# Optimization experiments

Measured on AMD Instinct MI355X. Metric: run time of the kernel, lower is better.

The kernel has to match this reference:

```python
import jax, jax.numpy as jnp
import numpy as np

H = 1024      # hidden_size
NH = 16       # num_heads
DK = H // NH  # head dim


def setup_inputs() -> dict:
    key = jax.random.key(0)
    ks = jax.random.split(key, 5)
    s = 0.02
    return {
        "x": jax.random.normal(ks[0], (4, 2048, H), dtype=jnp.float32),
        "W_attn": jax.random.normal(ks[1], (H, 3 * H), dtype=jnp.float32) * s,
        "b_attn": jnp.zeros((3 * H,), dtype=jnp.float32),
        "W_proj": jax.random.normal(ks[2], (H, H), dtype=jnp.float32) * s,
        "b_proj": jnp.zeros((H,), dtype=jnp.float32),
    }


def reference(x, W_attn, b_attn, W_proj, b_proj):
    B, S, _ = x.shape
    qkv = x @ W_attn + b_attn                      # [B,S,3H]
    q, k, v = jnp.split(qkv, 3, axis=-1)
    # split heads -> [B,NH,S,DK]
    def heads(t):
        return t.reshape(B, S, NH, DK).transpose(0, 2, 1, 3)
    q, k, v = heads(q), heads(k), heads(v)
    scores = jnp.einsum("bhqd,bhkd->bhqk", q, k) / jnp.sqrt(jnp.float32(DK))
    causal = jnp.triu(jnp.full((S, S), -jnp.inf, dtype=scores.dtype), k=1)
    scores = scores + causal                        # additive causal mask
    attn = jax.nn.softmax(scores, axis=-1)
    out = jnp.einsum("bhqk,bhkd->bhqd", attn, v)   # [B,NH,S,DK]
    out = out.transpose(0, 2, 1, 3).reshape(B, S, H)
    return out @ W_proj + b_proj
```

## Files before the change

### kernel.cpp

```cpp
#include <hip/hip_runtime.h>
#include <hip/hip_bf16.h>


typedef __attribute__((ext_vector_type(8))) short bhalf8;
typedef __attribute__((ext_vector_type(4))) float floatx4;
typedef __attribute__((ext_vector_type(16))) float floatx16;

#define SB 2048
#define HB 1024
#define H3 3072

#if __has_builtin(__builtin_amdgcn_exp2f)
#define EXP2(x) __builtin_amdgcn_exp2f(x)
#else
#define EXP2(x) exp2f(x)
#endif

__device__ __forceinline__ float bf2f(unsigned short u) {
  union { unsigned int i; float f; } c; c.i = ((unsigned int)u) << 16; return c.f;
}
__device__ __forceinline__ unsigned short f2bf(float f) {
  union { float f; unsigned int i; } c; c.f = f;
  unsigned int r = c.i + 0x7fffu + ((c.i >> 16) & 1u);
  return (unsigned short)(r >> 16);
}
__device__ __forceinline__ int pkbf(float lo, float hi_) {
  union { __hip_bfloat162 h; int i; } u;
  u.h = __float22bfloat162_rn(make_float2(lo, hi_));
  return u.i;
}

__device__ __forceinline__ void gl_lds16(const unsigned short* g, unsigned short* l) {
  __builtin_amdgcn_global_load_lds(
      (const __attribute__((address_space(1))) unsigned int*)g,
      (__attribute__((address_space(3))) unsigned int*)l, 16, 0, 0);
}

#define REP16(OP) OP(0) OP(1) OP(2) OP(3) OP(4) OP(5) OP(6) OP(7) \
                  OP(8) OP(9) OP(10) OP(11) OP(12) OP(13) OP(14) OP(15)

__global__ void cvt_f32_bf16(const float* __restrict__ in, unsigned short* __restrict__ out, int n) {
  int i = (blockIdx.x * blockDim.x + threadIdx.x) * 4;
  if (i >= n) return;
  float4 v = *(const float4*)(in + i);
  ushort4 o;
  o.x = f2bf(v.x); o.y = f2bf(v.y); o.z = f2bf(v.z); o.w = f2bf(v.w);
  *(ushort4*)(out + i) = o;
}

__global__ void transpose_cvt(const float* __restrict__ in, unsigned short* __restrict__ out,
                              int K, int N) {
  __shared__ float tile[32][33];
  int n0 = blockIdx.x * 32, k0 = blockIdx.y * 32;
  for (int i = threadIdx.y; i < 32; i += 8)
    tile[i][threadIdx.x] = in[(size_t)(k0 + i) * N + n0 + threadIdx.x];
  __syncthreads();
  for (int i = threadIdx.y; i < 32; i += 8)
    out[(size_t)(n0 + i) * K + k0 + threadIdx.x] = f2bf(tile[threadIdx.x][i]);
}

__global__ void transpose_v(const unsigned short* __restrict__ qkv,
                            unsigned short* __restrict__ Vt) {
  __shared__ unsigned short tile[32][33];
  const int bh = blockIdx.z;
  const int b = bh >> 4, h = bh & 15;
  const int s0 = blockIdx.x * 32;
  const int d0 = blockIdx.y * 32;
  const int tx = threadIdx.x;
  const unsigned short* src = qkv + (size_t)(b * SB + s0) * H3 + 2 * HB + h * 64 + d0;
  for (int i = threadIdx.y; i < 32; i += 8)
    tile[i][tx] = src[(size_t)i * H3 + tx];
  __syncthreads();
  unsigned short* dst = Vt + ((size_t)bh * 64 + d0) * SB + s0;
  for (int i = threadIdx.y; i < 32; i += 8)
    dst[(size_t)i * SB + tx] = tile[tx][i];
}

__global__ __launch_bounds__(512, 2) void gemm_v8(
    const unsigned short* __restrict__ A,
    const unsigned short* __restrict__ Bt,
    const float* __restrict__ bias,
    unsigned short* __restrict__ C,
    int M, int N, int K) {
  __shared__ __align__(16) unsigned short Sm[3 * 20480];
  const int tid = threadIdx.x;
  const int lane = tid & 63;
  const int w = tid >> 6;
  const int l15 = lane & 15, l4 = lane >> 4;
  const int wm = w >> 2, wn = w & 3;

  const int gx = gridDim.x;
  int lin = blockIdx.y * gx + blockIdx.x;
  const int cpx = (gx * gridDim.y) >> 3;
  lin = (lin & 7) * cpx + (lin >> 3);
  const int m0 = (lin / gx) * 256;
  const int n0 = (lin % gx) * 384;

  const int rb0 = tid >> 2;
  const int co = (((tid & 3) ^ ((tid >> 3) & 3)) * 8);
  const unsigned short* pA0 = A + (size_t)(m0 + rb0) * K + co;
  const unsigned short* pA1 = pA0 + (size_t)128 * K;
  const unsigned short* pB0 = Bt + (size_t)(n0 + rb0) * K + co;
  const unsigned short* pB1 = pB0 + (size_t)128 * K;
  const unsigned short* pB2 = pB0 + (size_t)256 * K;

  const int ra0 = wm * 128 + l15;
  const int ab0 = ra0 * 64 + ((l4 ^ ((ra0 >> 1) & 3)) << 4);
  const int rbq = wn * 96 + l15;
  const int bb0 = 16384 + rbq * 64 + ((l4 ^ ((rbq >> 1) & 3)) << 4);

  const floatx4 zero = {0.f, 0.f, 0.f, 0.f};
  floatx4 acc[8][6];
#pragma unroll
  for (int i = 0; i < 8; ++i)
#pragma unroll
    for (int j = 0; j < 6; ++j) acc[i][j] = zero;

#define STAGE_A(k0, ss)                                                 \
  { gl_lds16(pA0 + (k0), Sm + (ss) + tid * 8);                          \
    gl_lds16(pA1 + (k0), Sm + (ss) + (tid + 512) * 8); }
#define STAGE_B(k0, ss)                                                 \
  { gl_lds16(pB0 + (k0), Sm + (ss) + 8192 + tid * 8);                   \
    gl_lds16(pB1 + (k0), Sm + (ss) + 8192 + (tid + 512) * 8);           \
    gl_lds16(pB2 + (k0), Sm + (ss) + 8192 + (tid + 1024) * 8); }

  const int NT = K >> 5;
  STAGE_A(0, 0)      STAGE_B(0, 0)
  STAGE_A(32, 20480) STAGE_B(32, 20480)
  int sb = 0;
  int ss = 40960;

  for (int t = 0; t < NT; ++t) {
    if (t < NT - 1) asm volatile("s_waitcnt vmcnt(5)" ::: "memory");
    else            asm volatile("s_waitcnt vmcnt(0)" ::: "memory");
    __builtin_amdgcn_s_barrier();

    const char* LB = (const char*)(Sm + sb);
    const int k2 = (t + 2) * 32;
    const bool st = (t + 2 < NT);

    bhalf8 a0 = *(const bhalf8*)(LB + ab0);
    bhalf8 a1 = *(const bhalf8*)(LB + ab0 + 1024);
    bhalf8 a2 = *(const bhalf8*)(LB + ab0 + 2048);
    bhalf8 a3 = *(const bhalf8*)(LB + ab0 + 3072);
    bhalf8 b0 = *(const bhalf8*)(LB + bb0);
    bhalf8 b1 = *(const bhalf8*)(LB + bb0 + 1024);
    bhalf8 b2 = *(const bhalf8*)(LB + bb0 + 2048);
    bhalf8 b3 = *(const bhalf8*)(LB + bb0 + 3072);
    bhalf8 b4 = *(const bhalf8*)(LB + bb0 + 4096);
    bhalf8 b5 = *(const bhalf8*)(LB + bb0 + 5120);
    if (st) STAGE_A(k2, ss)
    asm volatile("s_waitcnt lgkmcnt(0)" ::: "memory");
    __builtin_amdgcn_sched_barrier(0);
    __builtin_amdgcn_s_setprio(1);
#define MROW(i, av)                                                              \
    acc[i][0] = __builtin_amdgcn_mfma_f32_16x16x32_bf16(av, b0, acc[i][0], 0, 0, 0); \
    acc[i][1] = __builtin_amdgcn_mfma_f32_16x16x32_bf16(av, b1, acc[i][1], 0, 0, 0); \
    acc[i][2] = __builtin_amdgcn_mfma_f32_16x16x32_bf16(av, b2, acc[i][2], 0, 0, 0); \
    acc[i][3] = __builtin_amdgcn_mfma_f32_16x16x32_bf16(av, b3, acc[i][3], 0, 0, 0); \
    acc[i][4] = __builtin_amdgcn_mfma_f32_16x16x32_bf16(av, b4, acc[i][4], 0, 0, 0); \
    acc[i][5] = __builtin_amdgcn_mfma_f32_16x16x32_bf16(av, b5, acc[i][5], 0, 0, 0);
    MROW(0, a0) MROW(1, a1) MROW(2, a2) MROW(3, a3)
    __builtin_amdgcn_s_setprio(0);
    __builtin_amdgcn_sched_barrier(0);
    __builtin_amdgcn_s_barrier();

    bhalf8 a4 = *(const bhalf8*)(LB + ab0 + 4096);
    bhalf8 a5 = *(const bhalf8*)(LB + ab0 + 5120);
    bhalf8 a6 = *(const bhalf8*)(LB + ab0 + 6144);
    bhalf8 a7 = *(const bhalf8*)(LB + ab0 + 7168);
    if (st) STAGE_B(k2, ss)
    asm volatile("s_waitcnt lgkmcnt(0)" ::: "memory");
    __builtin_amdgcn_sched_barrier(0);
    __builtin_amdgcn_s_setprio(1);
    MROW(4, a4) MROW(5, a5) MROW(6, a6) MROW(7, a7)
#undef MROW
    __builtin_amdgcn_s_setprio(0);
    __builtin_amdgcn_sched_barrier(0);
    __builtin_amdgcn_s_barrier();

    sb = (sb == 40960) ? 0 : sb + 20480;
    ss = (ss == 40960) ? 0 : ss + 20480;
  }
#undef STAGE_A
#undef STAGE_B

#pragma unroll
  for (int i = 0; i < 8; ++i) {
    int row = m0 + wm * 128 + i * 16 + (l4 << 2);
#pragma unroll
    for (int j = 0; j < 6; ++j) {
      int col = n0 + wn * 96 + j * 16 + l15;
      float bb = bias[col];
#pragma unroll
      for (int r = 0; r < 4; ++r)
        C[(size_t)(row + r) * N + col] = f2bf(acc[i][j][r] + bb);
    }
  }
}

template <bool F32OUT>
__global__ __launch_bounds__(512, 4) void gemm_v6(
    const unsigned short* __restrict__ A,
    const unsigned short* __restrict__ Bt,
    const float* __restrict__ bias,
    void* __restrict__ Cv,
    int M, int N, int K) {
  __shared__ __align__(16) unsigned short Sm[3 * 12288];
  const int tid = threadIdx.x;
  const int lane = tid & 63;
  const int w = tid >> 6;
  const int l15 = lane & 15, l4 = lane >> 4;
  const int wr = (w >> 1) * 64;
  const int wc = (w & 1) * 64;

  const int gx = gridDim.x;
  int lin = blockIdx.y * gx + blockIdx.x;
  const int cpx = (gx * gridDim.y) >> 3;
  lin = (lin & 7) * cpx + (lin >> 3);
  const int m0 = (lin / gx) * 256;
  const int n0 = (lin % gx) * 128;

  const int idx0 = tid, idx1 = tid + 512;
  const unsigned short* pA0 = A + (size_t)(m0 + (idx0 >> 2)) * K + (((idx0 & 3) ^ ((idx0 >> 3) & 3)) * 8);
  const unsigned short* pA1 = A + (size_t)(m0 + (idx1 >> 2)) * K + (((idx1 & 3) ^ ((idx1 >> 3) & 3)) * 8);
  const unsigned short* pB  = Bt + (size_t)(n0 + (tid >> 2)) * K + (((tid & 3) ^ ((tid >> 3) & 3)) * 8);

  int abyte[4], bbyte[4];
#pragma unroll
  for (int i = 0; i < 4; ++i) {
    int ra = wr + i * 16 + l15;
    abyte[i] = ra * 64 + ((l4 ^ ((ra >> 1) & 3)) << 4);
    int rb = wc + i * 16 + l15;
    bbyte[i] = 16384 + rb * 64 + ((l4 ^ ((rb >> 1) & 3)) << 4);
  }

  const floatx4 zero = {0.f, 0.f, 0.f, 0.f};
  floatx4 acc[4][4];
#pragma unroll
  for (int i = 0; i < 4; ++i)
#pragma unroll
    for (int j = 0; j < 4; ++j) acc[i][j] = zero;

#define STAGE_A6(k0, sbase)                                             \
  { gl_lds16(pA0 + (k0), Sm + (sbase) + idx0 * 8);                      \
    gl_lds16(pA1 + (k0), Sm + (sbase) + idx1 * 8); }
#define STAGE_B6(k0, sbase)                                             \
  { gl_lds16(pB + (k0), Sm + (sbase) + 8192 + tid * 8); }

  const int NT = K >> 5;
  STAGE_A6(0, 0)  STAGE_B6(0, 0)
  STAGE_A6(32, 12288) STAGE_B6(32, 12288)
  int sb = 0;
  int ss = 24576;

  for (int t = 0; t < NT; ++t) {
    if (t < NT - 1) asm volatile("s_waitcnt vmcnt(3)" ::: "memory");
    else            asm volatile("s_waitcnt vmcnt(0)" ::: "memory");
    __builtin_amdgcn_s_barrier();

    const char* LB = (const char*)(Sm + sb);
    const int k2 = (t + 2) * 32;
    const bool st = (t + 2 < NT);

    bhalf8 a0 = *(const bhalf8*)(LB + abyte[0]);
    bhalf8 a1 = *(const bhalf8*)(LB + abyte[1]);
    bhalf8 b0 = *(const bhalf8*)(LB + bbyte[0]);
    bhalf8 b1 = *(const bhalf8*)(LB + bbyte[1]);
    bhalf8 b2 = *(const bhalf8*)(LB + bbyte[2]);
    bhalf8 b3 = *(const bhalf8*)(LB + bbyte[3]);
    if (st) STAGE_A6(k2, ss)
    asm volatile("s_waitcnt lgkmcnt(0)" ::: "memory");
    __builtin_amdgcn_sched_barrier(0);
    __builtin_amdgcn_s_setprio(1);
    acc[0][0] = __builtin_amdgcn_mfma_f32_16x16x32_bf16(a0, b0, acc[0][0], 0, 0, 0);
    acc[0][1] = __builtin_amdgcn_mfma_f32_16x16x32_bf16(a0, b1, acc[0][1], 0, 0, 0);
    acc[0][2] = __builtin_amdgcn_mfma_f32_16x16x32_bf16(a0, b2, acc[0][2], 0, 0, 0);
    acc[0][3] = __builtin_amdgcn_mfma_f32_16x16x32_bf16(a0, b3, acc[0][3], 0, 0, 0);
    acc[1][0] = __builtin_amdgcn_mfma_f32_16x16x32_bf16(a1, b0, acc[1][0], 0, 0, 0);
    acc[1][1] = __builtin_amdgcn_mfma_f32_16x16x32_bf16(a1, b1, acc[1][1], 0, 0, 0);
    acc[1][2] = __builtin_amdgcn_mfma_f32_16x16x32_bf16(a1, b2, acc[1][2], 0, 0, 0);
    acc[1][3] = __builtin_amdgcn_mfma_f32_16x16x32_bf16(a1, b3, acc[1][3], 0, 0, 0);
    __builtin_amdgcn_s_setprio(0);
    __builtin_amdgcn_sched_barrier(0);
    __builtin_amdgcn_s_barrier();

    bhalf8 a2 = *(const bhalf8*)(LB + abyte[2]);
    bhalf8 a3 = *(const bhalf8*)(LB + abyte[3]);
    if (st) STAGE_B6(k2, ss)
    asm volatile("s_waitcnt lgkmcnt(0)" ::: "memory");
    __builtin_amdgcn_sched_barrier(0);
    __builtin_amdgcn_s_setprio(1);
    acc[2][0] = __builtin_amdgcn_mfma_f32_16x16x32_bf16(a2, b0, acc[2][0], 0, 0, 0);
    acc[2][1] = __builtin_amdgcn_mfma_f32_16x16x32_bf16(a2, b1, acc[2][1], 0, 0, 0);
    acc[2][2] = __builtin_amdgcn_mfma_f32_16x16x32_bf16(a2, b2, acc[2][2], 0, 0, 0);
    acc[2][3] = __builtin_amdgcn_mfma_f32_16x16x32_bf16(a2, b3, acc[2][3], 0, 0, 0);
    acc[3][0] = __builtin_amdgcn_mfma_f32_16x16x32_bf16(a3, b0, acc[3][0], 0, 0, 0);
    acc[3][1] = __builtin_amdgcn_mfma_f32_16x16x32_bf16(a3, b1, acc[3][1], 0, 0, 0);
    acc[3][2] = __builtin_amdgcn_mfma_f32_16x16x32_bf16(a3, b2, acc[3][2], 0, 0, 0);
    acc[3][3] = __builtin_amdgcn_mfma_f32_16x16x32_bf16(a3, b3, acc[3][3], 0, 0, 0);
    __builtin_amdgcn_s_setprio(0);
    __builtin_amdgcn_sched_barrier(0);
    __builtin_amdgcn_s_barrier();

    sb = (sb == 24576) ? 0 : sb + 12288;
    ss = (ss == 24576) ? 0 : ss + 12288;
  }
#undef STAGE_A6
#undef STAGE_B6

  float* Cf = (float*)Cv;
  unsigned short* Cb = (unsigned short*)Cv;
#pragma unroll
  for (int i = 0; i < 4; ++i) {
    int row = m0 + wr + i * 16 + (l4 << 2);
#pragma unroll
    for (int j = 0; j < 4; ++j) {
      int col = n0 + wc + j * 16 + l15;
      float bb = bias[col];
#pragma unroll
      for (int r = 0; r < 4; ++r) {
        float v = acc[i][j][r] + bb;
        size_t idx = (size_t)(row + r) * N + col;
        if constexpr (F32OUT) Cf[idx] = v;
        else Cb[idx] = f2bf(v);
      }
    }
  }
}

__global__ __launch_bounds__(256, 4) void flash_attn4(
    const unsigned short* __restrict__ qkv,
    const unsigned short* __restrict__ Vt,
    unsigned short* __restrict__ outp) {
  __shared__ __align__(16) unsigned short Sm[4 * 4096];

  const int tid = threadIdx.x;
  const int lane = tid & 63;
  const int w = tid >> 6;
  const int hi = lane >> 5;
  const int qc = lane & 31;
  const int bh = blockIdx.x;
  const int b = bh >> 4, h = bh & 15;
  const int qt = 15 - (int)blockIdx.y;
  const int wq0 = qt * 128 + w * 32;
  const size_t rowbase = (size_t)b * SB;
  const int qg = wq0 + qc;
  const int nt = 2 * qt + 2;

  bhalf8 qf[4];
  {
    const unsigned short* qp = qkv + (rowbase + qg) * H3 + h * 64 + hi * 8;
#pragma unroll
    for (int kk = 0; kk < 4; ++kk) {
      bhalf8 v = *(const bhalf8*)(qp + kk * 16);
      bhalf8 o;
#pragma unroll
      for (int j = 0; j < 8; ++j)
        o[j] = (short)f2bf(bf2f((unsigned short)v[j]) * 0.18033688f);
      qf[kk] = o;
    }
  }

  const floatx16 Z16 = {0,0,0,0,0,0,0,0,0,0,0,0,0,0,0,0};
  floatx16 acc0 = Z16, acc1 = Z16;
  float l_half = 0.f;

  const char* LB = (const char*)Sm;
  int koff[8];
#pragma unroll
  for (int kk = 0; kk < 4; ++kk) {
    int xo = (((2 * kk + hi) ^ (qc & 7)) << 4);
    koff[2 * kk]     = qc * 128 + xo;
    koff[2 * kk + 1] = (32 + qc) * 128 + xo;
  }

  const int srow = tid >> 3, schk = tid & 7;
  const int sxe = (schk ^ (srow & 7)) * 8;
  const unsigned short* kp = qkv + (rowbase + srow) * H3 + HB + h * 64 + sxe;
  const unsigned short* vp = Vt + ((size_t)bh * 64 + srow) * SB + sxe;

  {
    unsigned short* kb = Sm + tid * 8;
    gl_lds16(kp, kb);
    gl_lds16(kp + 32 * H3, kb + 2048);
    gl_lds16(vp, kb + 8192);
    gl_lds16(vp + 32 * SB, kb + 8192 + 2048);
  }

#define QKK(BUFB, kk)                                                              \
      { bhalf8 ka = *(const bhalf8*)(LB + (BUFB) + koff[2*(kk)]);                  \
        s0 = __builtin_amdgcn_mfma_f32_32x32x16_bf16(ka, qf[kk], s0, 0, 0, 0);     \
        bhalf8 kb2 = *(const bhalf8*)(LB + (BUFB) + koff[2*(kk)+1]);               \
        s1 = __builtin_amdgcn_mfma_f32_32x32x16_bf16(kb2, qf[kk], s1, 0, 0, 0); }
#define PVC(BUFB, c, pfv)                                                          \
      { bhalf8 va = *(const bhalf8*)(LB + 16384 + (BUFB) + koff[2*(c)]);           \
        acc0 = __builtin_amdgcn_mfma_f32_32x32x16_bf16(va, pfv, acc0, 0, 0, 0);    \
        bhalf8 vb2 = *(const bhalf8*)(LB + 16384 + (BUFB) + koff[2*(c)+1]);        \
        acc1 = __builtin_amdgcn_mfma_f32_32x32x16_bf16(vb2, pfv, acc1, 0, 0, 0); }
#define MSK0(r) { if (k0 + (((r)&3) + 8*((r)>>2)) + 4*hi > qg)      s0[r] = -3.0e38f; }
#define MSK1(r) { if (k0 + 32 + (((r)&3) + 8*((r)>>2)) + 4*hi > qg) s1[r] = -3.0e38f; }
#define PEXP(r) { s0[r] = EXP2(s0[r]); s1[r] = EXP2(s1[r]); rsx[(r)&3] += s0[r] + s1[r]; }
  union PW { int i[4]; bhalf8 v; };
#define PACK2(dst, sv, rb)                                               \
      { int A0 = pkbf(sv[rb + 0], sv[rb + 1]);                           \
        int A1 = pkbf(sv[rb + 2], sv[rb + 3]);                           \
        int B0 = pkbf(sv[rb + 4], sv[rb + 5]);                           \
        int B1 = pkbf(sv[rb + 6], sv[rb + 7]);                           \
        auto r0 = __builtin_amdgcn_permlane32_swap(A0, B0, false, false);\
        auto r1 = __builtin_amdgcn_permlane32_swap(A1, B1, false, false);\
        PW u;                                                            \
        u.i[0] = r0[0]; u.i[1] = r1[0];                                  \
        u.i[2] = r0[1]; u.i[3] = r1[1];                                  \
        dst = u.v; }

#define FLASH_COMPUTE(BUFB)                                                        \
    { floatx16 s0 = Z16, s1 = Z16;                                                 \
      __builtin_amdgcn_s_setprio(1);                                               \
      QKK(BUFB, 0) QKK(BUFB, 1) QKK(BUFB, 2) QKK(BUFB, 3)                          \
      __builtin_amdgcn_s_setprio(0);                                               \
      if (k0 + 63 > wq0) { REP16(MSK0) REP16(MSK1) }                               \
      float rsx[4] = {0.f, 0.f, 0.f, 0.f};                                         \
      REP16(PEXP)                                                                  \
      l_half += (rsx[0] + rsx[1]) + (rsx[2] + rsx[3]);                             \
      bhalf8 pf0, pf1, pf2, pf3;                                                   \
      PACK2(pf0, s0, 0) PACK2(pf1, s0, 8) PACK2(pf2, s1, 0) PACK2(pf3, s1, 8)      \
      __builtin_amdgcn_s_setprio(1);                                               \
      PVC(BUFB, 0, pf0) PVC(BUFB, 1, pf1) PVC(BUFB, 2, pf2) PVC(BUFB, 3, pf3)      \
      __builtin_amdgcn_s_setprio(0); }

#define DO_STEP(T, BUF)                                                            \
  { __syncthreads();                                                               \
    if ((T) + 1 < nt) {                                                            \
      kp += 64 * H3; vp += 64;                                                     \
      unsigned short* kb = Sm + (1 - (BUF)) * 4096 + tid * 8;                      \
      gl_lds16(kp, kb); gl_lds16(kp + 32 * H3, kb + 2048);                         \
      gl_lds16(vp, kb + 8192); gl_lds16(vp + 32 * SB, kb + 8192 + 2048);           \
    }                                                                              \
    const int k0 = (T) * 64;                                                       \
    if (k0 <= wq0 + 31) FLASH_COMPUTE((BUF) * 8192)                                \
  }

  for (int t = 0; t < nt; t += 2) {
    DO_STEP(t, 0)
    DO_STEP(t + 1, 1)
  }

  const float l_full = l_half + __shfl_xor(l_half, 32);
  const float inv_l = 1.f / l_full;
  unsigned short* op = outp + (rowbase + qg) * HB + h * 64;
#pragma unroll
  for (int tq = 0; tq < 4; ++tq) {
    ushort4 st;
    st.x = f2bf(acc0[4 * tq + 0] * inv_l);
    st.y = f2bf(acc0[4 * tq + 1] * inv_l);
    st.z = f2bf(acc0[4 * tq + 2] * inv_l);
    st.w = f2bf(acc0[4 * tq + 3] * inv_l);
    *(ushort4*)(op + 8 * tq + 4 * hi) = st;
    ushort4 su;
    su.x = f2bf(acc1[4 * tq + 0] * inv_l);
    su.y = f2bf(acc1[4 * tq + 1] * inv_l);
    su.z = f2bf(acc1[4 * tq + 2] * inv_l);
    su.w = f2bf(acc1[4 * tq + 3] * inv_l);
    *(ushort4*)(op + 32 + 8 * tq + 4 * hi) = su;
  }
}

extern "C" void kernel_launch(void* const* d_in, const int* in_sizes, int n_in,
                              void* d_out, int out_size, void* d_ws, size_t ws_size,
                              hipStream_t stream) {
  const float* x      = (const float*)d_in[0];
  const float* W_attn = (const float*)d_in[1];
  const float* b_attn = (const float*)d_in[2];
  const float* W_proj = (const float*)d_in[3];
  const float* b_proj = (const float*)d_in[4];
  float* out = (float*)d_out;

  char* ws = (char*)d_ws;
  unsigned short* x_bf    = (unsigned short*)(ws);
  unsigned short* Wt_attn = (unsigned short*)(ws + 16777216);
  unsigned short* Wt_proj = (unsigned short*)(ws + 23068672);
  unsigned short* qkv     = (unsigned short*)(ws + 25165824);
  unsigned short* attn    = (unsigned short*)(ws + 75497472);
  unsigned short* Vt      = x_bf;

  cvt_f32_bf16<<<8192, 256, 0, stream>>>(x, x_bf, 8192 * 1024);
  transpose_cvt<<<dim3(96, 32), dim3(32, 8), 0, stream>>>(W_attn, Wt_attn, 1024, 3072);
  transpose_cvt<<<dim3(32, 32), dim3(32, 8), 0, stream>>>(W_proj, Wt_proj, 1024, 1024);

  gemm_v8<<<dim3(8, 32), 512, 0, stream>>>(x_bf, Wt_attn, b_attn, qkv,
                                           8192, 3072, 1024);
  transpose_v<<<dim3(64, 2, 64), dim3(32, 8), 0, stream>>>(qkv, Vt);
  flash_attn4<<<dim3(64, 16), 256, 0, stream>>>(qkv, Vt, attn);
  gemm_v6<true><<<dim3(8, 32), 512, 0, stream>>>(attn, Wt_proj, b_proj, out,
                                                 8192, 1024, 1024);
}
```

Measured before the change: 153.3 us.

## Fuse V transpose into QKV GEMM epilogue and trim per-iteration barriers

The QKV GEMM epilogue now writes the V third of its output straight into the transposed Vt layout in a separate workspace region, so the standalone transpose_v kernel is skipped whenever the workspace is large enough. Separately, both GEMM main loops drop the explicit lgkmcnt waits, the sched_barriers, and the trailing s_barrier of each iteration. The goal is to save a launch plus a read and write of V, and to reduce synchronisation stalls. The cost is scattered 8-byte stores into Vt. Removing the trailing barrier risks a race where the next iteration's async staging overwrites an LDS buffer that other waves are still reading, though the triple buffering may cover this.

```diff
diff --git a/kernel.cpp b/kernel.cpp
--- a/kernel.cpp
+++ b/kernel.cpp
@@ -76,11 +76,13 @@
     dst[(size_t)i * SB + tx] = tile[tx][i];
 }
 
-__global__ __launch_bounds__(512, 2) void gemm_v8(
+template <bool FUSEV>
+__global__ __launch_bounds__(512, 2) void gemm_v9(
     const unsigned short* __restrict__ A,
     const unsigned short* __restrict__ Bt,
     const float* __restrict__ bias,
     unsigned short* __restrict__ C,
+    unsigned short* __restrict__ Vt,
     int M, int N, int K) {
   __shared__ __align__(16) unsigned short Sm[3 * 20480];
   const int tid = threadIdx.x;
@@ -150,8 +152,6 @@
     bhalf8 b4 = *(const bhalf8*)(LB + bb0 + 4096);
     bhalf8 b5 = *(const bhalf8*)(LB + bb0 + 5120);
     if (st) STAGE_A(k2, ss)
-    asm volatile("s_waitcnt lgkmcnt(0)" ::: "memory");
-    __builtin_amdgcn_sched_barrier(0);
     __builtin_amdgcn_s_setprio(1);
 #define MROW(i, av)                                                              \
     acc[i][0] = __builtin_amdgcn_mfma_f32_16x16x32_bf16(av, b0, acc[i][0], 0, 0, 0); \
@@ -162,7 +162,6 @@
     acc[i][5] = __builtin_amdgcn_mfma_f32_16x16x32_bf16(av, b5, acc[i][5], 0, 0, 0);
     MROW(0, a0) MROW(1, a1) MROW(2, a2) MROW(3, a3)
     __builtin_amdgcn_s_setprio(0);
-    __builtin_amdgcn_sched_barrier(0);
     __builtin_amdgcn_s_barrier();
 
     bhalf8 a4 = *(const bhalf8*)(LB + ab0 + 4096);
@@ -170,14 +169,10 @@
     bhalf8 a6 = *(const bhalf8*)(LB + ab0 + 6144);
     bhalf8 a7 = *(const bhalf8*)(LB + ab0 + 7168);
     if (st) STAGE_B(k2, ss)
-    asm volatile("s_waitcnt lgkmcnt(0)" ::: "memory");
-    __builtin_amdgcn_sched_barrier(0);
     __builtin_amdgcn_s_setprio(1);
     MROW(4, a4) MROW(5, a5) MROW(6, a6) MROW(7, a7)
 #undef MROW
     __builtin_amdgcn_s_setprio(0);
-    __builtin_amdgcn_sched_barrier(0);
-    __builtin_amdgcn_s_barrier();
 
     sb = (sb == 40960) ? 0 : sb + 20480;
     ss = (ss == 40960) ? 0 : ss + 20480;
@@ -192,9 +187,21 @@
     for (int j = 0; j < 6; ++j) {
       int col = n0 + wn * 96 + j * 16 + l15;
       float bb = bias[col];
-#pragma unroll
-      for (int r = 0; r < 4; ++r)
-        C[(size_t)(row + r) * N + col] = f2bf(acc[i][j][r] + bb);
+      if (!FUSEV || col < 2048) {
+#pragma unroll
+        for (int r = 0; r < 4; ++r)
+          C[(size_t)(row + r) * N + col] = f2bf(acc[i][j][r] + bb);
+      } else {
+        int vc = col - 2048;
+        int h = vc >> 6, dk = vc & 63;
+        int b = row >> 11, s = row & 2047;
+        ushort4 pv;
+        pv.x = f2bf(acc[i][j][0] + bb);
+        pv.y = f2bf(acc[i][j][1] + bb);
+        pv.z = f2bf(acc[i][j][2] + bb);
+        pv.w = f2bf(acc[i][j][3] + bb);
+        *(ushort4*)(Vt + ((size_t)((b * 16 + h) * 64 + dk)) * SB + s) = pv;
+      }
     }
   }
 }
@@ -270,8 +277,6 @@
     bhalf8 b2 = *(const bhalf8*)(LB + bbyte[2]);
     bhalf8 b3 = *(const bhalf8*)(LB + bbyte[3]);
     if (st) STAGE_A6(k2, ss)
-    asm volatile("s_waitcnt lgkmcnt(0)" ::: "memory");
-    __builtin_amdgcn_sched_barrier(0);
     __builtin_amdgcn_s_setprio(1);
     acc[0][0] = __builtin_amdgcn_mfma_f32_16x16x32_bf16(a0, b0, acc[0][0], 0, 0, 0);
     acc[0][1] = __builtin_amdgcn_mfma_f32_16x16x32_bf16(a0, b1, acc[0][1], 0, 0, 0);
@@ -282,14 +287,11 @@
     acc[1][2] = __builtin_amdgcn_mfma_f32_16x16x32_bf16(a1, b2, acc[1][2], 0, 0, 0);
     acc[1][3] = __builtin_amdgcn_mfma_f32_16x16x32_bf16(a1, b3, acc[1][3], 0, 0, 0);
     __builtin_amdgcn_s_setprio(0);
-    __builtin_amdgcn_sched_barrier(0);
     __builtin_amdgcn_s_barrier();
 
     bhalf8 a2 = *(const bhalf8*)(LB + abyte[2]);
     bhalf8 a3 = *(const bhalf8*)(LB + abyte[3]);
     if (st) STAGE_B6(k2, ss)
-    asm volatile("s_waitcnt lgkmcnt(0)" ::: "memory");
-    __builtin_amdgcn_sched_barrier(0);
     __builtin_amdgcn_s_setprio(1);
     acc[2][0] = __builtin_amdgcn_mfma_f32_16x16x32_bf16(a2, b0, acc[2][0], 0, 0, 0);
     acc[2][1] = __builtin_amdgcn_mfma_f32_16x16x32_bf16(a2, b1, acc[2][1], 0, 0, 0);
@@ -300,8 +302,6 @@
     acc[3][2] = __builtin_amdgcn_mfma_f32_16x16x32_bf16(a3, b2, acc[3][2], 0, 0, 0);
     acc[3][3] = __builtin_amdgcn_mfma_f32_16x16x32_bf16(a3, b3, acc[3][3], 0, 0, 0);
     __builtin_amdgcn_s_setprio(0);
-    __builtin_amdgcn_sched_barrier(0);
-    __builtin_amdgcn_s_barrier();
 
     sb = (sb == 24576) ? 0 : sb + 12288;
     ss = (ss == 24576) ? 0 : ss + 12288;
@@ -482,15 +482,22 @@
   unsigned short* Wt_proj = (unsigned short*)(ws + 23068672);
   unsigned short* qkv     = (unsigned short*)(ws + 25165824);
   unsigned short* attn    = (unsigned short*)(ws + 75497472);
-  unsigned short* Vt      = x_bf;
+  const bool fuse = ws_size >= (size_t)92274688 + 16777216;
+  unsigned short* VtF = (unsigned short*)(ws + 92274688);
+  unsigned short* Vt  = fuse ? VtF : x_bf;
 
   cvt_f32_bf16<<<8192, 256, 0, stream>>>(x, x_bf, 8192 * 1024);
   transpose_cvt<<<dim3(96, 32), dim3(32, 8), 0, stream>>>(W_attn, Wt_attn, 1024, 3072);
   transpose_cvt<<<dim3(32, 32), dim3(32, 8), 0, stream>>>(W_proj, Wt_proj, 1024, 1024);
 
-  gemm_v8<<<dim3(8, 32), 512, 0, stream>>>(x_bf, Wt_attn, b_attn, qkv,
-                                           8192, 3072, 1024);
-  transpose_v<<<dim3(64, 2, 64), dim3(32, 8), 0, stream>>>(qkv, Vt);
+  if (fuse) {
+    gemm_v9<true><<<dim3(8, 32), 512, 0, stream>>>(x_bf, Wt_attn, b_attn, qkv, VtF,
+                                                   8192, 3072, 1024);
+  } else {
+    gemm_v9<false><<<dim3(8, 32), 512, 0, stream>>>(x_bf, Wt_attn, b_attn, qkv, nullptr,
+                                                    8192, 3072, 1024);
+    transpose_v<<<dim3(64, 2, 64), dim3(32, 8), 0, stream>>>(qkv, Vt);
+  }
   flash_attn4<<<dim3(64, 16), 256, 0, stream>>>(qkv, Vt, attn);
   gemm_v6<true><<<dim3(8, 32), 512, 0, stream>>>(attn, Wt_proj, b_proj, out,
                                                  8192, 1024, 1024);
```

Result: faster. 145.9 us (-4.8%).
